# Performance work log

Measured on AMD Instinct MI355X. Metric: run time of the kernel, lower is better.

The kernel has to match this reference:

```python
import jax, jax.numpy as jnp
import numpy as np

B, N, DIM = 4, 4096, 1024
HEADS, DIM_HEAD = 16, 64
DIM_INNER = HEADS * DIM_HEAD
ATTN_SCALE = 8.0
EPS = 1e-12  # F.normalize default eps


def setup_inputs() -> dict:
    key = jax.random.key(0)
    k1, k2, k3, k4, k5 = jax.random.split(key, 5)
    x = jax.random.normal(k1, (B, N, DIM), dtype=jnp.float32)
    gamma = jnp.ones((DIM,), dtype=jnp.float32)
    # stored as (in, out) so forward is x @ w
    w_qkv = jax.random.normal(k2, (DIM, 3 * DIM_INNER), dtype=jnp.float32) * (DIM ** -0.5)
    temperature = jnp.ones((HEADS, 1, 1), dtype=jnp.float32)
    w_out = jax.random.normal(k3, (DIM_INNER, DIM), dtype=jnp.float32) * (DIM_INNER ** -0.5)
    return {"x": x, "gamma": gamma, "w_qkv": w_qkv, "temperature": temperature, "w_out": w_out}


def _l2norm(t):
    # F.normalize(t, dim=-1): t / max(||t||_2, eps)
    n = jnp.linalg.norm(t, axis=-1, keepdims=True)
    return t / jnp.maximum(n, EPS)


def reference(x, gamma, w_qkv, temperature, w_out):
    b, n, dim = x.shape
    # RMSNorm: F.normalize(x, dim=-1) * sqrt(dim) * gamma
    xn = _l2norm(x) * (dim ** 0.5) * gamma
    # QKV projection -> qkv b h d n
    qkv = (xn @ w_qkv).reshape(b, n, 3, HEADS, DIM_HEAD)
    qkv = qkv.transpose(2, 0, 3, 4, 1)  # (3, b, h, d, n)
    q, k, v = qkv[0], qkv[1], qkv[2]
    # l2-normalize q, k over the sequence (last) axis; temperature-scale q
    q = _l2norm(q) * jnp.exp(temperature)  # temperature: (h,1,1) broadcast
    k = _l2norm(k)
    # cross-covariance attention over the small channel dim d
    sim = jnp.einsum('bhdn,bhen->bhde', q, k) * ATTN_SCALE
    attn = jax.nn.softmax(sim, axis=-1)
    out = jnp.einsum('bhde,bhen->bhdn', attn, v)
    # b h d n -> b n (h d), then out projection
    out = out.transpose(0, 3, 1, 2).reshape(b, n, DIM_INNER)
    return out @ w_out
```

## Files before the change

kernel.cpp:

```cpp
#include <hip/hip_runtime.h>
#include <stdint.h>

typedef unsigned short u16;
typedef unsigned int u32;
typedef __attribute__((ext_vector_type(8))) __bf16 bf16x8;
typedef __attribute__((ext_vector_type(4))) float f32x4;

#define M_TOT 16384
#define DIMX  1024

__device__ __forceinline__ u16 f2b(float f) {
  u32 u = __builtin_bit_cast(u32, f);
  u32 r = (u + 0x7fffu + ((u >> 16) & 1u)) >> 16;
  return (u16)r;
}

__device__ __forceinline__ void gl2lds16(const void* g, void* l) {
  __builtin_amdgcn_global_load_lds((const __attribute__((address_space(1))) void*)g,
                                   (__attribute__((address_space(3))) void*)l,
                                   16, 0, 0);
}

__global__ __launch_bounds__(256) void k_rms(const float* __restrict__ x,
                                             const float* __restrict__ gamma,
                                             u16* __restrict__ xn) {
  int row = blockIdx.x;
  int t = threadIdx.x;
  const float4* xr = (const float4*)(x + (size_t)row * DIMX);
  float4 v = xr[t];
  float ss = v.x * v.x + v.y * v.y + v.z * v.z + v.w * v.w;
#pragma unroll
  for (int o = 32; o > 0; o >>= 1) ss += __shfl_xor(ss, o, 64);
  __shared__ float wss[4];
  int w = t >> 6;
  if ((t & 63) == 0) wss[w] = ss;
  __syncthreads();
  float tot = wss[0] + wss[1] + wss[2] + wss[3];
  float scale = 32.0f / fmaxf(sqrtf(tot), 1e-12f);
  float4 g = ((const float4*)gamma)[t];
  ushort4 o4;
  o4.x = f2b(v.x * scale * g.x);
  o4.y = f2b(v.y * scale * g.y);
  o4.z = f2b(v.z * scale * g.z);
  o4.w = f2b(v.w * scale * g.w);
  ((ushort4*)xn)[(size_t)row * 256 + t] = o4;
}

__global__ __launch_bounds__(256) void k_castT(const float* __restrict__ in,
                                               u16* __restrict__ out, int Rr, int Cc) {
  __shared__ float tile[32][33];
  int c0 = blockIdx.x * 32, r0 = blockIdx.y * 32;
  int tx = threadIdx.x, ty = threadIdx.y;
#pragma unroll
  for (int i = 0; i < 4; i++)
    tile[ty + i * 8][tx] = in[(size_t)(r0 + ty + i * 8) * Cc + c0 + tx];
  __syncthreads();
#pragma unroll
  for (int i = 0; i < 4; i++)
    out[(size_t)(c0 + ty + i * 8) * Rr + r0 + tx] = f2b(tile[tx][ty + i * 8]);
}


template<bool SWAP>
__device__ __forceinline__ f32x4 mf(bf16x8 a, bf16x8 b, f32x4 c) {
  return SWAP ? __builtin_amdgcn_mfma_f32_16x16x32_bf16(b, a, c, 0, 0, 0)
              : __builtin_amdgcn_mfma_f32_16x16x32_bf16(a, b, c, 0, 0, 0);
}

__device__ __forceinline__ void stage_half(const u16* __restrict__ g,
                                           u16* dst, int t, int k0) {
#pragma unroll
  for (int r = 0; r < 2; r++) {
    int chunk = r * 512 + t;
    int row = chunk >> 3;
    int cc = (chunk & 7) ^ (row & 7);
    gl2lds16(g + (size_t)row * 1024 + (k0 + cc * 8),
             dst + (r * 512 + (t >> 6) * 64) * 8);
  }
}

template<bool SWAP>
__device__ __forceinline__ void gemm_core256(const u16* __restrict__ Ag,
                                             const u16* __restrict__ Bg,
                                             u16* lds, int t, f32x4 (&acc)[8][4]) {
  const int lane = t & 63;
  const int r16 = lane & 15, q = lane >> 4;
  const int s0 = (q ^ (r16 & 7)) * 8;
  const int wr = (t >> 6) >> 2, wc = (t >> 6) & 3;
  const int arow = wr * 16 + r16;
  const int brow = wc * 16 + r16;

  stage_half(Ag,              lds + 0,     t, 0);
  stage_half(Bg,              lds + 16384, t, 0);
  stage_half(Bg + 128 * 1024, lds + 24576, t, 0);
  stage_half(Ag + 128 * 1024, lds + 8192,  t, 0);
  stage_half(Ag,              lds + 32768 + 0,     t, 64);
  stage_half(Bg,              lds + 32768 + 16384, t, 64);
  stage_half(Bg + 128 * 1024, lds + 32768 + 24576, t, 64);
  asm volatile("s_waitcnt vmcnt(6)" ::: "memory");
  __builtin_amdgcn_s_barrier();

  bf16x8 af[4][2], bl[2][2], bh[2][2];
#pragma unroll 1
  for (int tt = 0; tt < 16; tt++) {
    const int bo = (tt & 1) << 15;
    const int nb = bo ^ 32768;
    const int k1 = ((tt + 1) & 15) << 6;
    const int k2 = ((tt + 2) & 15) << 6;
    const u16* A0 = lds + bo;
    const u16* A1 = lds + bo + 8192;
    const u16* B0 = lds + bo + 16384;
    const u16* B1 = lds + bo + 24576;

#pragma unroll
    for (int i = 0; i < 4; i++) {
      af[i][0] = *(const bf16x8*)(A0 + (i * 32 + arow) * 64 + s0);
      af[i][1] = *(const bf16x8*)(A0 + (i * 32 + arow) * 64 + (s0 ^ 32));
    }
#pragma unroll
    for (int j = 0; j < 2; j++) {
      bl[j][0] = *(const bf16x8*)(B0 + (j * 64 + brow) * 64 + s0);
      bl[j][1] = *(const bf16x8*)(B0 + (j * 64 + brow) * 64 + (s0 ^ 32));
    }
    stage_half(Ag + 128 * 1024, lds + nb + 8192, t, k1);
    __builtin_amdgcn_s_barrier();
    asm volatile("s_waitcnt lgkmcnt(0)" ::: "memory");
    __builtin_amdgcn_s_setprio(1);
#pragma unroll
    for (int kq = 0; kq < 2; kq++)
#pragma unroll
      for (int i = 0; i < 4; i++)
#pragma unroll
        for (int j = 0; j < 2; j++)
          acc[i][j] = mf<SWAP>(af[i][kq], bl[j][kq], acc[i][j]);
    __builtin_amdgcn_s_setprio(0);
    __builtin_amdgcn_s_barrier();

#pragma unroll
    for (int j = 0; j < 2; j++) {
      bh[j][0] = *(const bf16x8*)(B1 + (j * 64 + brow) * 64 + s0);
      bh[j][1] = *(const bf16x8*)(B1 + (j * 64 + brow) * 64 + (s0 ^ 32));
    }
    stage_half(Ag, lds + bo, t, k2);
    __builtin_amdgcn_s_barrier();
    asm volatile("s_waitcnt lgkmcnt(0)" ::: "memory");
    __builtin_amdgcn_s_setprio(1);
#pragma unroll
    for (int kq = 0; kq < 2; kq++)
#pragma unroll
      for (int i = 0; i < 4; i++)
#pragma unroll
        for (int j = 0; j < 2; j++)
          acc[i][2 + j] = mf<SWAP>(af[i][kq], bh[j][kq], acc[i][2 + j]);
    __builtin_amdgcn_s_setprio(0);
    __builtin_amdgcn_s_barrier();

#pragma unroll
    for (int i = 0; i < 4; i++) {
      af[i][0] = *(const bf16x8*)(A1 + (i * 32 + arow) * 64 + s0);
      af[i][1] = *(const bf16x8*)(A1 + (i * 32 + arow) * 64 + (s0 ^ 32));
    }
    stage_half(Bg, lds + bo + 16384, t, k2);
    __builtin_amdgcn_s_barrier();
    asm volatile("s_waitcnt lgkmcnt(0)" ::: "memory");
    __builtin_amdgcn_s_setprio(1);
#pragma unroll
    for (int kq = 0; kq < 2; kq++)
#pragma unroll
      for (int i = 0; i < 4; i++)
#pragma unroll
        for (int j = 0; j < 2; j++)
          acc[4 + i][j] = mf<SWAP>(af[i][kq], bl[j][kq], acc[4 + i][j]);
    __builtin_amdgcn_s_setprio(0);
    __builtin_amdgcn_s_barrier();

    stage_half(Bg + 128 * 1024, lds + bo + 24576, t, k2);
    __builtin_amdgcn_s_setprio(1);
#pragma unroll
    for (int kq = 0; kq < 2; kq++)
#pragma unroll
      for (int i = 0; i < 4; i++)
#pragma unroll
        for (int j = 0; j < 2; j++)
          acc[4 + i][2 + j] = mf<SWAP>(af[i][kq], bh[j][kq], acc[4 + i][2 + j]);
    __builtin_amdgcn_s_setprio(0);
    asm volatile("s_waitcnt vmcnt(6)" ::: "memory");
    __builtin_amdgcn_s_barrier();
  }
}

__global__ __launch_bounds__(512, 2) void k_gemm1(const u16* __restrict__ A,
                                                  const u16* __restrict__ Bt,
                                                  u16* __restrict__ qkT,
                                                  u16* __restrict__ vmat,
                                                  float* __restrict__ sumsq) {
  __shared__ u16 lds[8 * 8192];
  int l = blockIdx.x;
  int xcd = l & 7, c = l >> 3;
  int mt = xcd * 8 + (c & 7);
  int nt = c >> 3;
  int m0 = mt * 256, n0 = nt * 256;
  int t = threadIdx.x, lane = t & 63;
  int r16 = lane & 15, q = lane >> 4;
  int wr = (t >> 6) >> 2, wc = (t >> 6) & 3;
  f32x4 acc[8][4] = {};
  if (n0 < 2048) {
    gemm_core256<false>(A + (size_t)m0 * 1024, Bt + (size_t)n0 * 1024, lds, t, acc);
    int b = m0 >> 12;
#pragma unroll
    for (int j = 0; j < 4; j++) {
      int cc = n0 + j * 64 + wc * 16 + r16;
      float colss = 0.f;
#pragma unroll
      for (int i = 0; i < 8; i++) {
        f32x4 a = acc[i][j];
        colss += a.x * a.x + a.y * a.y + a.z * a.z + a.w * a.w;
        int m = m0 + i * 32 + wr * 16 + q * 4;
        ushort4 o4;
        o4.x = f2b(a.x); o4.y = f2b(a.y); o4.z = f2b(a.z); o4.w = f2b(a.w);
        *(ushort4*)(qkT + (size_t)cc * M_TOT + m) = o4;
      }
      colss += __shfl_xor(colss, 16, 64);
      colss += __shfl_xor(colss, 32, 64);
      if (lane < 16) atomicAdd(&sumsq[b * 2048 + cc], colss);
    }
  } else {
    gemm_core256<true>(A + (size_t)m0 * 1024, Bt + (size_t)n0 * 1024, lds, t, acc);
    int vc0 = n0 - 2048;
#pragma unroll
    for (int i = 0; i < 8; i++) {
      int m = m0 + i * 32 + wr * 16 + r16;
#pragma unroll
      for (int j = 0; j < 4; j++) {
        int cc = vc0 + j * 64 + wc * 16 + q * 4;
        f32x4 a = acc[i][j];
        ushort4 o4;
        o4.x = f2b(a.x); o4.y = f2b(a.y); o4.z = f2b(a.z); o4.w = f2b(a.w);
        *(ushort4*)(vmat + (size_t)m * 1024 + cc) = o4;
      }
    }
  }
}

__global__ __launch_bounds__(256) void k_attn_s(const u16* __restrict__ qkT,
                                                float* __restrict__ Spart) {
  int g = blockIdx.x, split = blockIdx.y;
  int t = threadIdx.x, lane = t & 63, w = t >> 6;
  int bh = g * 4 + w;
  int b = bh >> 4, h = bh & 15;
  int r16 = lane & 15, q = lane >> 4;
  const u16* qbase = qkT + (size_t)(h * 64) * M_TOT + b * 4096;
  const u16* kbase = qkT + (size_t)(1024 + h * 64) * M_TOT + b * 4096;
  f32x4 acc[4][4] = {};
#pragma unroll
  for (int it = 0; it < 8; it++) {
    int kk = split * 256 + it * 32 + q * 8;
    bf16x8 af[4], bfr[4];
#pragma unroll
    for (int i = 0; i < 4; i++) af[i] = *(const bf16x8*)(qbase + (size_t)(i * 16 + r16) * M_TOT + kk);
#pragma unroll
    for (int j = 0; j < 4; j++) bfr[j] = *(const bf16x8*)(kbase + (size_t)(j * 16 + r16) * M_TOT + kk);
#pragma unroll
    for (int i = 0; i < 4; i++)
#pragma unroll
      for (int j = 0; j < 4; j++)
        acc[i][j] = __builtin_amdgcn_mfma_f32_16x16x32_bf16(bfr[j], af[i], acc[i][j], 0, 0, 0);
  }
  float* Sp = Spart + ((size_t)split * 64 + bh) * 4096;
#pragma unroll
  for (int i = 0; i < 4; i++) {
    int d = i * 16 + r16;
#pragma unroll
    for (int j = 0; j < 4; j++) {
      int e = j * 16 + q * 4;
      *(f32x4*)(Sp + d * 64 + e) = acc[i][j];
    }
  }
}

__global__ __launch_bounds__(256) void k_softmax(const float* __restrict__ Spart,
                                                 const float* __restrict__ sumsq,
                                                 const float* __restrict__ temp,
                                                 u16* __restrict__ PT) {
  int bh = blockIdx.x;
  int b = bh >> 4, h = bh & 15;
  int t = threadIdx.x;
  int d = t & 63, w = t >> 6;
  int e0 = w * 16;
  __shared__ float rnk[64];
  __shared__ float redm[4][64];
  __shared__ float reds[4][64];
  if (t < 64) rnk[t] = 1.0f / fmaxf(sqrtf(sumsq[b * 2048 + 1024 + h * 64 + t]), 1e-12f);
  __syncthreads();
  float nq = sqrtf(sumsq[b * 2048 + h * 64 + d]);
  float qs = 8.0f * __expf(temp[h]) / fmaxf(nq, 1e-12f);
  const float* Sp = Spart + (size_t)bh * 4096 + d * 64 + e0;
  float vals[16];
#pragma unroll
  for (int e = 0; e < 16; e += 4) {
    f32x4 v = {};
#pragma unroll
    for (int s = 0; s < 16; s++)
      v += *(const f32x4*)(Sp + (size_t)s * 64 * 4096 + e);
    vals[e + 0] = v.x; vals[e + 1] = v.y; vals[e + 2] = v.z; vals[e + 3] = v.w;
  }
  float mx = -3.0e38f;
#pragma unroll
  for (int e = 0; e < 16; e++) {
    float v = vals[e] * qs * rnk[e0 + e];
    vals[e] = v;
    mx = fmaxf(mx, v);
  }
  redm[w][d] = mx;
  __syncthreads();
  float M = fmaxf(fmaxf(redm[0][d], redm[1][d]), fmaxf(redm[2][d], redm[3][d]));
  float s = 0.f;
#pragma unroll
  for (int e = 0; e < 16; e++) {
    float v = __expf(vals[e] - M);
    vals[e] = v;
    s += v;
  }
  reds[w][d] = s;
  __syncthreads();
  float inv = 1.0f / (reds[0][d] + reds[1][d] + reds[2][d] + reds[3][d]);
#pragma unroll
  for (int e = 0; e < 16; e++)
    PT[((size_t)bh * 64 + e0 + e) * 64 + d] = f2b(vals[e] * inv);
}

__global__ __launch_bounds__(256) void k_m(const u16* __restrict__ woT,
                                           const u16* __restrict__ PT,
                                           u16* __restrict__ MT) {
  int bh = blockIdx.x;
  int b = bh >> 4, h = bh & 15;
  int o0 = blockIdx.y * 128;
  int t = threadIdx.x, lane = t & 63, w = t >> 6;
  int r16 = lane & 15, q = lane >> 4;
  const u16* pbase = PT + (size_t)bh * 4096;
  f32x4 acc[2][4] = {};
#pragma unroll
  for (int ks = 0; ks < 2; ks++) {
    int kk = ks * 32 + q * 8;
    bf16x8 af[2], bfr[4];
#pragma unroll
    for (int i = 0; i < 2; i++)
      af[i] = *(const bf16x8*)(woT + (size_t)(o0 + w * 32 + i * 16 + r16) * 1024 + h * 64 + kk);
#pragma unroll
    for (int j = 0; j < 4; j++)
      bfr[j] = *(const bf16x8*)(pbase + (size_t)(j * 16 + r16) * 64 + kk);
#pragma unroll
    for (int i = 0; i < 2; i++)
#pragma unroll
      for (int j = 0; j < 4; j++)
        acc[i][j] = __builtin_amdgcn_mfma_f32_16x16x32_bf16(af[i], bfr[j], acc[i][j], 0, 0, 0);
  }
  u16* dst = MT + (size_t)b * 1024 * 1024;
#pragma unroll
  for (int i = 0; i < 2; i++) {
    int o = o0 + w * 32 + i * 16 + q * 4;
#pragma unroll
    for (int j = 0; j < 4; j++) {
      int e = h * 64 + j * 16 + r16;
      f32x4 a = acc[i][j];
      dst[(size_t)(o + 0) * 1024 + e] = f2b(a.x);
      dst[(size_t)(o + 1) * 1024 + e] = f2b(a.y);
      dst[(size_t)(o + 2) * 1024 + e] = f2b(a.z);
      dst[(size_t)(o + 3) * 1024 + e] = f2b(a.w);
    }
  }
}

__global__ __launch_bounds__(512, 2) void k_gemm2(const u16* __restrict__ A,
                                                  const u16* __restrict__ Bt,
                                                  float* __restrict__ C) {
  __shared__ u16 lds[8 * 8192];
  int l = blockIdx.x;
  int xcd = l & 7, c = l >> 3;
  int mt = xcd * 8 + (c & 7);
  int nt = c >> 3;
  int m0 = mt * 256, n0 = nt * 256;
  int b = m0 >> 12;
  const u16* Bb = Bt + (size_t)b * 1024 * 1024;
  int t = threadIdx.x, lane = t & 63;
  int r16 = lane & 15, q = lane >> 4;
  int wr = (t >> 6) >> 2, wc = (t >> 6) & 3;
  f32x4 acc[8][4] = {};
  gemm_core256<true>(A + (size_t)m0 * 1024, Bb + (size_t)n0 * 1024, lds, t, acc);
#pragma unroll
  for (int i = 0; i < 8; i++) {
    int m = m0 + i * 32 + wr * 16 + r16;
#pragma unroll
    for (int j = 0; j < 4; j++) {
      int cc = n0 + j * 64 + wc * 16 + q * 4;
      *(f32x4*)(C + (size_t)m * 1024 + cc) = acc[i][j];
    }
  }
}

extern "C" void kernel_launch(void* const* d_in, const int* in_sizes, int n_in,
                              void* d_out, int out_size, void* d_ws, size_t ws_size,
                              hipStream_t stream) {
  const float* x     = (const float*)d_in[0];
  const float* gamma = (const float*)d_in[1];
  const float* wqkv  = (const float*)d_in[2];
  const float* temp  = (const float*)d_in[3];
  const float* wout  = (const float*)d_in[4];
  float* out = (float*)d_out;

  char* ws = (char*)d_ws;
  size_t off = 0;
  u16* xn = (u16*)(ws + off);    off += (size_t)M_TOT * 1024 * 2;
  u16* wqT = (u16*)(ws + off);   off += (size_t)3072 * 1024 * 2;
  u16* woT = (u16*)(ws + off);   off += (size_t)1024 * 1024 * 2;
  u16* qkT = (u16*)(ws + off);   off += (size_t)2048 * M_TOT * 2;
  u16* vmat = (u16*)(ws + off);  off += (size_t)M_TOT * 1024 * 2;
  float* sumsq = (float*)(ws + off); off += (size_t)4 * 2048 * 4;
  u16* PT = (u16*)(ws + off);    off += (size_t)64 * 64 * 64 * 2;
  u16* MT = (u16*)(ws + off);    off += (size_t)4 * 1024 * 1024 * 2;

  float* Spart = (float*)xn;

  hipMemsetAsync((void*)sumsq, 0, (size_t)4 * 2048 * 4, stream);

  k_rms<<<16384, 256, 0, stream>>>(x, gamma, xn);
  dim3 cb(32, 8);
  k_castT<<<dim3(3072 / 32, 1024 / 32), cb, 0, stream>>>(wqkv, wqT, 1024, 3072);
  k_castT<<<dim3(1024 / 32, 1024 / 32), cb, 0, stream>>>(wout, woT, 1024, 1024);
  k_gemm1<<<768, 512, 0, stream>>>(xn, wqT, qkT, vmat, sumsq);
  k_attn_s<<<dim3(16, 16), 256, 0, stream>>>(qkT, Spart);
  k_softmax<<<64, 256, 0, stream>>>(Spart, sumsq, temp, PT);
  k_m<<<dim3(64, 8), 256, 0, stream>>>(woT, PT, MT);
  k_gemm2<<<1024 / 4, 512, 0, stream>>>(vmat, MT, out);
}
```

Baseline: 329.0 us.

## Rework GEMM prefetch schedule and restage attention-sim kernel through LDS

The GEMM main loop now prefetches only one k-step ahead into the alternate buffer, in place of the previous two-ahead scheme. It drops several barriers and lgkmcnt waits and uses a uniform vmcnt(4) wait before each barrier. Separately, the q·kᵀ kernel switches from one wave per head with direct global loads to one block per (batch, head) with swizzled global-to-LDS staging of 64x256 tiles, and 4 sequence splits instead of 16. The softmax partial-sum loop is reduced to match. The aim is fewer barriers in the GEMM and more coalesced, LDS-reused loads in the sim kernel, at the risk of less latency hiding in the GEMM and fewer blocks in the sim kernel.

```diff
diff --git a/kernel.cpp b/kernel.cpp
--- a/kernel.cpp
+++ b/kernel.cpp
@@ -94,10 +94,7 @@
   stage_half(Bg,              lds + 16384, t, 0);
   stage_half(Bg + 128 * 1024, lds + 24576, t, 0);
   stage_half(Ag + 128 * 1024, lds + 8192,  t, 0);
-  stage_half(Ag,              lds + 32768 + 0,     t, 64);
-  stage_half(Bg,              lds + 32768 + 16384, t, 64);
-  stage_half(Bg + 128 * 1024, lds + 32768 + 24576, t, 64);
-  asm volatile("s_waitcnt vmcnt(6)" ::: "memory");
+  asm volatile("s_waitcnt vmcnt(4)" ::: "memory");
   __builtin_amdgcn_s_barrier();
 
   bf16x8 af[4][2], bl[2][2], bh[2][2];
@@ -106,7 +103,6 @@
     const int bo = (tt & 1) << 15;
     const int nb = bo ^ 32768;
     const int k1 = ((tt + 1) & 15) << 6;
-    const int k2 = ((tt + 2) & 15) << 6;
     const u16* A0 = lds + bo;
     const u16* A1 = lds + bo + 8192;
     const u16* B0 = lds + bo + 16384;
@@ -122,9 +118,7 @@
       bl[j][0] = *(const bf16x8*)(B0 + (j * 64 + brow) * 64 + s0);
       bl[j][1] = *(const bf16x8*)(B0 + (j * 64 + brow) * 64 + (s0 ^ 32));
     }
-    stage_half(Ag + 128 * 1024, lds + nb + 8192, t, k1);
-    __builtin_amdgcn_s_barrier();
-    asm volatile("s_waitcnt lgkmcnt(0)" ::: "memory");
+    stage_half(Ag, lds + nb, t, k1);
     __builtin_amdgcn_s_setprio(1);
 #pragma unroll
     for (int kq = 0; kq < 2; kq++)
@@ -134,6 +128,7 @@
         for (int j = 0; j < 2; j++)
           acc[i][j] = mf<SWAP>(af[i][kq], bl[j][kq], acc[i][j]);
     __builtin_amdgcn_s_setprio(0);
+    asm volatile("s_waitcnt vmcnt(4)" ::: "memory");
     __builtin_amdgcn_s_barrier();
 
 #pragma unroll
@@ -141,9 +136,7 @@
       bh[j][0] = *(const bf16x8*)(B1 + (j * 64 + brow) * 64 + s0);
       bh[j][1] = *(const bf16x8*)(B1 + (j * 64 + brow) * 64 + (s0 ^ 32));
     }
-    stage_half(Ag, lds + bo, t, k2);
-    __builtin_amdgcn_s_barrier();
-    asm volatile("s_waitcnt lgkmcnt(0)" ::: "memory");
+    stage_half(Bg, lds + nb + 16384, t, k1);
     __builtin_amdgcn_s_setprio(1);
 #pragma unroll
     for (int kq = 0; kq < 2; kq++)
@@ -153,6 +146,7 @@
         for (int j = 0; j < 2; j++)
           acc[i][2 + j] = mf<SWAP>(af[i][kq], bh[j][kq], acc[i][2 + j]);
     __builtin_amdgcn_s_setprio(0);
+    asm volatile("s_waitcnt vmcnt(4)" ::: "memory");
     __builtin_amdgcn_s_barrier();
 
 #pragma unroll
@@ -160,9 +154,7 @@
       af[i][0] = *(const bf16x8*)(A1 + (i * 32 + arow) * 64 + s0);
       af[i][1] = *(const bf16x8*)(A1 + (i * 32 + arow) * 64 + (s0 ^ 32));
     }
-    stage_half(Bg, lds + bo + 16384, t, k2);
-    __builtin_amdgcn_s_barrier();
-    asm volatile("s_waitcnt lgkmcnt(0)" ::: "memory");
+    stage_half(Bg + 128 * 1024, lds + nb + 24576, t, k1);
     __builtin_amdgcn_s_setprio(1);
 #pragma unroll
     for (int kq = 0; kq < 2; kq++)
@@ -174,7 +166,7 @@
     __builtin_amdgcn_s_setprio(0);
     __builtin_amdgcn_s_barrier();
 
-    stage_half(Bg + 128 * 1024, lds + bo + 24576, t, k2);
+    stage_half(Ag + 128 * 1024, lds + nb + 8192, t, k1);
     __builtin_amdgcn_s_setprio(1);
 #pragma unroll
     for (int kq = 0; kq < 2; kq++)
@@ -184,7 +176,7 @@
         for (int j = 0; j < 2; j++)
           acc[4 + i][2 + j] = mf<SWAP>(af[i][kq], bh[j][kq], acc[4 + i][2 + j]);
     __builtin_amdgcn_s_setprio(0);
-    asm volatile("s_waitcnt vmcnt(6)" ::: "memory");
+    asm volatile("s_waitcnt vmcnt(4)" ::: "memory");
     __builtin_amdgcn_s_barrier();
   }
 }
@@ -244,38 +236,47 @@
 
 __global__ __launch_bounds__(256) void k_attn_s(const u16* __restrict__ qkT,
                                                 float* __restrict__ Spart) {
-  int g = blockIdx.x, split = blockIdx.y;
+  __shared__ u16 Ql[64 * 256];
+  __shared__ u16 Kl[64 * 256];
+  int bh = blockIdx.x, split = blockIdx.y;
+  int b = bh >> 4, h = bh & 15;
   int t = threadIdx.x, lane = t & 63, w = t >> 6;
-  int bh = g * 4 + w;
-  int b = bh >> 4, h = bh & 15;
   int r16 = lane & 15, q = lane >> 4;
-  const u16* qbase = qkT + (size_t)(h * 64) * M_TOT + b * 4096;
-  const u16* kbase = qkT + (size_t)(1024 + h * 64) * M_TOT + b * 4096;
-  f32x4 acc[4][4] = {};
-#pragma unroll
-  for (int it = 0; it < 8; it++) {
-    int kk = split * 256 + it * 32 + q * 8;
-    bf16x8 af[4], bfr[4];
-#pragma unroll
-    for (int i = 0; i < 4; i++) af[i] = *(const bf16x8*)(qbase + (size_t)(i * 16 + r16) * M_TOT + kk);
-#pragma unroll
-    for (int j = 0; j < 4; j++) bfr[j] = *(const bf16x8*)(kbase + (size_t)(j * 16 + r16) * M_TOT + kk);
-#pragma unroll
-    for (int i = 0; i < 4; i++)
-#pragma unroll
-      for (int j = 0; j < 4; j++)
-        acc[i][j] = __builtin_amdgcn_mfma_f32_16x16x32_bf16(bfr[j], af[i], acc[i][j], 0, 0, 0);
+  const u16* qbase = qkT + (size_t)(h * 64) * M_TOT + b * 4096 + split * 1024;
+  const u16* kbase = qkT + (size_t)(1024 + h * 64) * M_TOT + b * 4096 + split * 1024;
+  int drow = w * 16 + r16;
+  f32x4 acc[4] = {};
+#pragma unroll 1
+  for (int it = 0; it < 4; it++) {
+    int ncol = it * 256;
+#pragma unroll
+    for (int r = 0; r < 8; r++) {
+      int ch = r * 256 + t;
+      int row = ch >> 5;
+      int sl = (ch & 31) ^ (row & 31);
+      gl2lds16(qbase + (size_t)row * M_TOT + ncol + sl * 8,
+               Ql + (r * 256 + w * 64) * 8);
+      gl2lds16(kbase + (size_t)row * M_TOT + ncol + sl * 8,
+               Kl + (r * 256 + w * 64) * 8);
+    }
+    asm volatile("s_waitcnt vmcnt(0)" ::: "memory");
+    __syncthreads();
+#pragma unroll
+    for (int it2 = 0; it2 < 8; it2++) {
+      bf16x8 aq = *(const bf16x8*)(Ql + drow * 256 + (((it2 * 4 + q) ^ (drow & 31)) * 8));
+#pragma unroll
+      for (int j = 0; j < 4; j++) {
+        int erow = j * 16 + r16;
+        bf16x8 bk = *(const bf16x8*)(Kl + erow * 256 + (((it2 * 4 + q) ^ (erow & 31)) * 8));
+        acc[j] = __builtin_amdgcn_mfma_f32_16x16x32_bf16(bk, aq, acc[j], 0, 0, 0);
+      }
+    }
+    __syncthreads();
   }
   float* Sp = Spart + ((size_t)split * 64 + bh) * 4096;
 #pragma unroll
-  for (int i = 0; i < 4; i++) {
-    int d = i * 16 + r16;
-#pragma unroll
-    for (int j = 0; j < 4; j++) {
-      int e = j * 16 + q * 4;
-      *(f32x4*)(Sp + d * 64 + e) = acc[i][j];
-    }
-  }
+  for (int j = 0; j < 4; j++)
+    *(f32x4*)(Sp + drow * 64 + j * 16 + q * 4) = acc[j];
 }
 
 __global__ __launch_bounds__(256) void k_softmax(const float* __restrict__ Spart,
@@ -300,7 +301,7 @@
   for (int e = 0; e < 16; e += 4) {
     f32x4 v = {};
 #pragma unroll
-    for (int s = 0; s < 16; s++)
+    for (int s = 0; s < 4; s++)
       v += *(const f32x4*)(Sp + (size_t)s * 64 * 4096 + e);
     vals[e + 0] = v.x; vals[e + 1] = v.y; vals[e + 2] = v.z; vals[e + 3] = v.w;
   }
@@ -428,7 +429,7 @@
   k_castT<<<dim3(3072 / 32, 1024 / 32), cb, 0, stream>>>(wqkv, wqT, 1024, 3072);
   k_castT<<<dim3(1024 / 32, 1024 / 32), cb, 0, stream>>>(wout, woT, 1024, 1024);
   k_gemm1<<<768, 512, 0, stream>>>(xn, wqT, qkT, vmat, sumsq);
-  k_attn_s<<<dim3(16, 16), 256, 0, stream>>>(qkT, Spart);
+  k_attn_s<<<dim3(64, 4), 256, 0, stream>>>(qkT, Spart);
   k_softmax<<<64, 256, 0, stream>>>(Spart, sumsq, temp, PT);
   k_m<<<dim3(64, 8), 256, 0, stream>>>(woT, PT, MT);
   k_gemm2<<<1024 / 4, 512, 0, stream>>>(vmat, MT, out);
```

Result: faster. 309.2 us (-6.0%).
